# Kernel tuning notes

Hardware: AMD Instinct MI355X
Metric: run time of the kernel (lower is better)

## Reference

```python
import jax, jax.numpy as jnp
import numpy as np


def setup_inputs() -> dict:
    key = jax.random.key(0)
    ks = jax.random.split(key, 5)
    B, T, I, H = 64, 512, 1024, 1024
    s = 1.0 / np.sqrt(H)
    return {
        "x": jax.random.normal(ks[0], (B, T, I), dtype=jnp.float32),
        "w_ih": jax.random.normal(ks[1], (4 * H, I), dtype=jnp.float32) * s,
        "b_ih": jax.random.normal(ks[2], (4 * H,), dtype=jnp.float32) * s,
        "w_hh": jax.random.normal(ks[3], (4 * H, H), dtype=jnp.float32) * s,
        "b_hh": jax.random.normal(ks[4], (4 * H,), dtype=jnp.float32) * s,
    }


def _lstm(x, w_ih, b_ih, w_hh, b_hh):
    B, T, _ = x.shape
    H = w_hh.shape[1]
    # Precompute input projections for all timesteps: [T, B, 4H]
    gx = jnp.einsum("bti,gi->tbg", x, w_ih) + b_ih
    h0 = jnp.zeros((B, H), dtype=x.dtype)
    c0 = jnp.zeros((B, H), dtype=x.dtype)

    def step(carry, g_x):
        h, c = carry
        gates = g_x + h @ w_hh.T + b_hh  # [B, 4H]
        i_lin, f_lin, g_lin, o_lin = jnp.split(gates, 4, axis=-1)
        i = jax.nn.sigmoid(i_lin)
        f = jax.nn.sigmoid(f_lin)
        g = jnp.tanh(g_lin)
        o = jax.nn.sigmoid(o_lin)
        c = f * c + i * g
        h = o * jnp.tanh(c)
        return (h, c), h

    (hT, cT), hs = jax.lax.scan(step, (h0, c0), gx)
    output = jnp.transpose(hs, (1, 0, 2))  # [B, T, H]
    hn = hT[None, :, :]  # [1, B, H]
    cn = cT[None, :, :]
    return output, hn, cn


def reference(x, w_ih, b_ih, w_hh, b_hh):
    return _lstm(x, w_ih, b_ih, w_hh, b_hh)
```

## Files before the change

### kernel.cpp

```cpp
#include <hip/hip_runtime.h>
#include <hip/hip_bf16.h>

#define Bv 64
#define Tv 512
#define Iv 1024
#define Hv 1024
#define G4v 4096
#define BH (Bv * Hv)
#define NHB 64
#define NXB 128
#define NBLK (NHB + NXB)
#define DEPTH 8
#define FSTR 16

typedef __attribute__((ext_vector_type(8))) short bf16x8;
typedef __attribute__((ext_vector_type(4))) float f32x4;

#define LOADC(p)    __hip_atomic_load((p), __ATOMIC_RELAXED, __HIP_MEMORY_SCOPE_AGENT)
#define STOREC(p,v) __hip_atomic_store((p), (v), __ATOMIC_RELAXED, __HIP_MEMORY_SCOPE_AGENT)

__device__ __forceinline__ float sigmoid_f(float v) { return 1.f / (1.f + __expf(-v)); }
__device__ __forceinline__ float tanh_f(float v) { return 1.f - 2.f / (__expf(2.f * v) + 1.f); }

__device__ __forceinline__ void store_short_sc1(void* p, unsigned short v) {
  asm volatile("global_store_short %0, %1, off sc1" :: "v"(p), "v"((unsigned)v) : "memory");
}

__global__ void prep(const float* __restrict__ w_ih, const float* __restrict__ w_hh,
                     const float* __restrict__ b_ih, const float* __restrict__ b_hh,
                     __hip_bfloat16* __restrict__ wbih, __hip_bfloat16* __restrict__ wbhh,
                     float* __restrict__ bias, __hip_bfloat16* __restrict__ hbuf,
                     unsigned* __restrict__ hflag, unsigned* __restrict__ xflag) {
  unsigned i = blockIdx.x * 256u + threadIdx.x;
  wbih[i] = __float2bfloat16(w_ih[i]);
  wbhh[i] = __float2bfloat16(w_hh[i]);
  if (i < (unsigned)G4v) bias[i] = b_ih[i] + b_hh[i];
  if (i < 2u * BH) hbuf[i] = __float2bfloat16(0.f);
  if (i < (unsigned)(4 * NHB * FSTR)) hflag[i] = 0u;
  if (i < (unsigned)(NXB * FSTR)) xflag[i] = 0u;
}

__global__ void __launch_bounds__(256, 1) lstm_main(
    const float* __restrict__ x,
    const __hip_bfloat16* __restrict__ wbih,
    const __hip_bfloat16* __restrict__ wbhh,
    const float* __restrict__ bias,
    __hip_bfloat16* __restrict__ hbuf,
    float* __restrict__ xg,
    float* __restrict__ out,
    unsigned* __restrict__ hflag,
    unsigned* __restrict__ xflag,
    int ring)
{
  extern __shared__ char lds[];

  const int bid  = blockIdx.x;
  const bool is_h = (bid < NHB);
  const int tid  = threadIdx.x;
  const int lane = tid & 63;
  const int wave = tid >> 6;
  const int lrow = lane & 15;
  const int lkg  = lane >> 4;
  const int lk   = lkg * 8;

  const int wg = is_h ? bid : ((bid - NHB) >> 1);
  const int rh = is_h ? 0 : ((bid - NHB) & 1);

  {
    const __hip_bfloat16* wsrc = is_h ? wbhh : wbih;
    for (int c = tid; c < 8192; c += 256) {
      int n   = c >> 7;
      int k16 = c & 127;
      int gc  = ((n >> 4) << 10) + (wg << 4) + (n & 15);
      uint4 v = *(const uint4*)(wsrc + ((size_t)gc << 10) + (k16 << 3));
      unsigned byt = (unsigned)((n << 11) + (k16 << 4)) ^ ((unsigned)(n & 7) << 4);
      *(uint4*)(&lds[byt]) = v;
    }
  }
  __syncthreads();

  if (!is_h) {
    const int j  = bid - NHB;
    const int wr = wave & 1;
    const int wc = wave >> 1;
    const int arow = rh * 32 + wr * 16 + lrow;
    const float* xa = x + (size_t)arow * (Tv * Iv) + lk;

    for (int t = 0; t < Tv; ++t) {
      if (t >= DEPTH) {
        if (wave == 0) {
          const unsigned tgt = (unsigned)(t - DEPTH + 1);
          for (;;) {
            unsigned a0 = LOADC(&hflag[(0 * 64 + lane) * FSTR]);
            unsigned a1 = LOADC(&hflag[(1 * 64 + lane) * FSTR]);
            unsigned a2 = LOADC(&hflag[(2 * 64 + lane) * FSTR]);
            unsigned a3 = LOADC(&hflag[(3 * 64 + lane) * FSTR]);
            if (__all(a0 >= tgt && a1 >= tgt && a2 >= tgt && a3 >= tgt)) break;
            __builtin_amdgcn_s_sleep(4);
          }
        }
        __syncthreads();
        asm volatile("" ::: "memory");
      }
      f32x4 acc[2];
      acc[0] = f32x4{0.f,0.f,0.f,0.f}; acc[1] = f32x4{0.f,0.f,0.f,0.f};
      const float* xt = xa + (size_t)t * Iv;
      #pragma unroll 4
      for (int ks = 0; ks < 32; ++ks) {
        int k0 = (ks << 5) + lk;
        float4 f0 = *(const float4*)(xt + (ks << 5));
        float4 f1 = *(const float4*)(xt + (ks << 5) + 4);
        union { __hip_bfloat16 e[8]; bf16x8 v; } u;
        u.e[0] = __float2bfloat16(f0.x); u.e[1] = __float2bfloat16(f0.y);
        u.e[2] = __float2bfloat16(f0.z); u.e[3] = __float2bfloat16(f0.w);
        u.e[4] = __float2bfloat16(f1.x); u.e[5] = __float2bfloat16(f1.y);
        u.e[6] = __float2bfloat16(f1.z); u.e[7] = __float2bfloat16(f1.w);
        bf16x8 b0, b1;
        {
          int n = wc * 32 + lrow;
          unsigned byt = (unsigned)((n << 11) + (k0 << 1)) ^ ((unsigned)(n & 7) << 4);
          b0 = *(const bf16x8*)(&lds[byt]);
          n += 16;
          byt = (unsigned)((n << 11) + (k0 << 1)) ^ ((unsigned)(n & 7) << 4);
          b1 = *(const bf16x8*)(&lds[byt]);
        }
        acc[0] = __builtin_amdgcn_mfma_f32_16x16x32_bf16(u.v, b0, acc[0], 0, 0, 0);
        acc[1] = __builtin_amdgcn_mfma_f32_16x16x32_bf16(u.v, b1, acc[1], 0, 0, 0);
      }
      float* dst = xg + (size_t)(t & (DEPTH - 1)) * (Bv * G4v);
      for (int nf = 0; nf < 2; ++nf) {
        int gc  = (wc * 2 + nf) * 1024 + (wg << 4) + lrow;
        int row = rh * 32 + wr * 16 + (lkg << 2);
        for (int r = 0; r < 4; ++r)
          STOREC(&dst[(size_t)(row + r) * G4v + gc], acc[nf][r]);
      }
      asm volatile("s_waitcnt vmcnt(0)" ::: "memory");
      __syncthreads();
      if (tid == 0) STOREC(&xflag[j * FSTR], (unsigned)(t + 1));
      __syncthreads();
    }
    return;
  }

  const int s     = wave;
  const int orow0 = s * 16 + (lkg << 2);
  const int ocol  = (wg << 4) + lrow;
  const int ar    = s * 16 + lrow;
  float c_state[4] = {0.f, 0.f, 0.f, 0.f};
  float biasv[4];
  #pragma unroll
  for (int g = 0; g < 4; ++g) biasv[g] = bias[(g << 10) + ocol];
  const unsigned* myxf = &xflag[(2 * wg + (s >> 1)) * FSTR];
  unsigned* myhf = &hflag[(s * 64 + wg) * FSTR];

  for (int t = 0; t < Tv; ++t) {
    for (;;) {
      unsigned hf = LOADC(&hflag[(s * 64 + lane) * FSTR]);
      unsigned xv = LOADC(myxf);
      if (__all(hf >= (unsigned)t && xv >= (unsigned)(t + 1))) break;
      __builtin_amdgcn_s_sleep(1);
    }
    asm volatile("" ::: "memory");
    f32x4 acc[4];
    for (int nf = 0; nf < 4; ++nf) acc[nf] = f32x4{0.f,0.f,0.f,0.f};
    bf16x8 aqv[32];
    if (ring) {
      const char* hrow = (const char*)(hbuf + (size_t)t * BH) + ((size_t)ar << 11) + (lkg << 4);
      #pragma unroll
      for (int ks = 0; ks < 32; ++ks)
        aqv[ks] = *(const bf16x8*)(hrow + (ks << 6));
    } else {
      const unsigned long long* hq =
          (const unsigned long long*)(hbuf + (size_t)(t & 1) * BH) + (size_t)ar * 256 + lkg * 2;
      #pragma unroll
      for (int ks = 0; ks < 32; ++ks) {
        union { unsigned long long q[2]; bf16x8 v; } ua;
        ua.q[0] = LOADC(hq + ks * 8);
        ua.q[1] = LOADC(hq + ks * 8 + 1);
        aqv[ks] = ua.v;
      }
    }
    float xgv[16];
    {
      const float* xgs = xg + (size_t)(t & (DEPTH - 1)) * (Bv * G4v);
      #pragma unroll
      for (int g = 0; g < 4; ++g)
        #pragma unroll
        for (int r = 0; r < 4; ++r)
          xgv[g * 4 + r] = LOADC(xgs + (size_t)(orow0 + r) * G4v + (g << 10) + ocol);
    }
    #pragma unroll
    for (int ks = 0; ks < 32; ++ks) {
      int k0 = (ks << 5) + lk;
      #pragma unroll
      for (int nf = 0; nf < 4; ++nf) {
        int n = nf * 16 + lrow;
        unsigned byt = (unsigned)((n << 11) + (k0 << 1)) ^ ((unsigned)(n & 7) << 4);
        bf16x8 b = *(const bf16x8*)(&lds[byt]);
        acc[nf] = __builtin_amdgcn_mfma_f32_16x16x32_bf16(aqv[ks], b, acc[nf], 0, 0, 0);
      }
    }
    float hv[4];
    #pragma unroll
    for (int r = 0; r < 4; ++r) {
      float g0 = acc[0][r] + xgv[0 + r]  + biasv[0];
      float g1 = acc[1][r] + xgv[4 + r]  + biasv[1];
      float g2 = acc[2][r] + xgv[8 + r]  + biasv[2];
      float g3 = acc[3][r] + xgv[12 + r] + biasv[3];
      float ig = sigmoid_f(g0);
      float fg = sigmoid_f(g1);
      float gg = tanh_f(g2);
      float og = sigmoid_f(g3);
      float cv = fg * c_state[r] + ig * gg;
      c_state[r] = cv;
      hv[r] = og * tanh_f(cv);
    }
    {
      __hip_bfloat16* hs = hbuf
          + (ring ? (size_t)(t + 1) * BH : (size_t)((t + 1) & 1) * BH) + ocol;
      #pragma unroll
      for (int r = 0; r < 4; ++r) {
        __hip_bfloat16 hb = __float2bfloat16(hv[r]);
        store_short_sc1(hs + ((size_t)(orow0 + r) << 10), *(unsigned short*)&hb);
      }
    }
    asm volatile("s_waitcnt vmcnt(0)" ::: "memory");
    if (lane == 0) STOREC(myhf, (unsigned)(t + 1));
    #pragma unroll
    for (int r = 0; r < 4; ++r) {
      float* ow = out + (size_t)(orow0 + r) * (Tv * Hv) + ((size_t)t << 10) + ocol;
      __builtin_nontemporal_store(hv[r], ow);
    }
    if (t == Tv - 1) {
      #pragma unroll
      for (int r = 0; r < 4; ++r) {
        float* hn = out + (size_t)Bv * Tv * Hv + ((size_t)(orow0 + r) << 10) + ocol;
        __builtin_nontemporal_store(hv[r], hn);
        __builtin_nontemporal_store(c_state[r], hn + BH);
      }
    }
  }
}

extern "C" void kernel_launch(void* const* d_in, const int* in_sizes, int n_in,
                              void* d_out, int out_size, void* d_ws, size_t ws_size,
                              hipStream_t stream) {
  const float* x    = (const float*)d_in[0];
  const float* w_ih = (const float*)d_in[1];
  const float* b_ih = (const float*)d_in[2];
  const float* w_hh = (const float*)d_in[3];
  const float* b_hh = (const float*)d_in[4];
  float* out = (float*)d_out;

  char* ws = (char*)d_ws;
  __hip_bfloat16* wbih = (__hip_bfloat16*)(ws);
  __hip_bfloat16* wbhh = (__hip_bfloat16*)(ws + ((size_t)8 << 20));
  float*          bias = (float*)(ws + ((size_t)16 << 20));
  float*          xg   = (float*)(ws + ((size_t)18 << 20));
  unsigned*       hflag= (unsigned*)(ws + ((size_t)26 << 20));
  unsigned*       xflag= (unsigned*)(ws + ((size_t)26 << 20) + 16384);

  const size_t ringBytes = (size_t)(Tv + 1) * BH * 2;
  const size_t needRing  = ((size_t)32 << 20) + ringBytes;
  const int ring = (ws_size >= needRing) ? 1 : 0;
  __hip_bfloat16* hbuf = ring
      ? (__hip_bfloat16*)(ws + ((size_t)32 << 20))
      : (__hip_bfloat16*)(ws + ((size_t)16 << 20) + 65536);

  hipLaunchKernelGGL(prep, dim3(16384), dim3(256), 0, stream,
                     w_ih, w_hh, b_ih, b_hh, wbih, wbhh, bias, hbuf, hflag, xflag);

  const unsigned ldsBytes = 131072u;
  hipFuncSetAttribute((const void*)lstm_main,
                      hipFuncAttributeMaxDynamicSharedMemorySize, (int)ldsBytes);

  const float* xA = x;
  const __hip_bfloat16* wbihA = wbih;
  const __hip_bfloat16* wbhhA = wbhh;
  const float* biasA = bias;
  __hip_bfloat16* hbufA = hbuf;
  float* xgA = xg;
  float* outA = out;
  unsigned* hflagA = hflag;
  unsigned* xflagA = xflag;
  int ringA = ring;
  void* args[10] = {(void*)&xA, (void*)&wbihA, (void*)&wbhhA, (void*)&biasA,
                    (void*)&hbufA, (void*)&xgA, (void*)&outA, (void*)&hflagA,
                    (void*)&xflagA, (void*)&ringA};

  hipError_t lerr = hipLaunchCooperativeKernel((const void*)lstm_main, dim3(NBLK),
                                               dim3(256), args, ldsBytes, stream);
  if (lerr != hipSuccess) {
    (void)hipGetLastError();
    hipLaunchKernelGGL(lstm_main, dim3(NBLK), dim3(256), ldsBytes, stream,
                       xA, wbihA, wbhhA, biasA, hbufA, xgA, outA, hflagA, xflagA, ringA);
  }
}
```

Before: 4.962 ms.

## Replace h-flag polling with sentinel-valued ring buffer data polling

```diff
diff --git a/kernel.cpp b/kernel.cpp
--- a/kernel.cpp
+++ b/kernel.cpp
@@ -12,6 +12,7 @@
 #define NBLK (NHB + NXB)
 #define DEPTH 8
 #define FSTR 16
+#define SENT 0xFF80u
 
 typedef __attribute__((ext_vector_type(8))) short bf16x8;
 typedef __attribute__((ext_vector_type(4))) float f32x4;
@@ -30,12 +31,21 @@
                      const float* __restrict__ b_ih, const float* __restrict__ b_hh,
                      __hip_bfloat16* __restrict__ wbih, __hip_bfloat16* __restrict__ wbhh,
                      float* __restrict__ bias, __hip_bfloat16* __restrict__ hbuf,
-                     unsigned* __restrict__ hflag, unsigned* __restrict__ xflag) {
+                     unsigned* __restrict__ hflag, unsigned* __restrict__ xflag, int ring) {
   unsigned i = blockIdx.x * 256u + threadIdx.x;
   wbih[i] = __float2bfloat16(w_ih[i]);
   wbhh[i] = __float2bfloat16(w_hh[i]);
   if (i < (unsigned)G4v) bias[i] = b_ih[i] + b_hh[i];
-  if (i < 2u * BH) hbuf[i] = __float2bfloat16(0.f);
+  if (ring) {
+    const unsigned NCH = (unsigned)(((size_t)(Tv + 1) * BH) / 8);
+    const uint4 sv = {SENT | (SENT << 16), SENT | (SENT << 16),
+                      SENT | (SENT << 16), SENT | (SENT << 16)};
+    for (unsigned j = i; j < NCH; j += 16384u * 256u)
+      ((uint4*)hbuf)[j] = sv;
+    if (i < (unsigned)(BH / 8)) ((uint4*)hbuf)[i] = uint4{0u, 0u, 0u, 0u};
+  } else {
+    if (i < 2u * BH) hbuf[i] = __float2bfloat16(0.f);
+  }
   if (i < (unsigned)(4 * NHB * FSTR)) hflag[i] = 0u;
   if (i < (unsigned)(NXB * FSTR)) xflag[i] = 0u;
 }
@@ -154,32 +164,53 @@
   unsigned* myhf = &hflag[(s * 64 + wg) * FSTR];
 
   for (int t = 0; t < Tv; ++t) {
-    for (;;) {
-      unsigned hf = LOADC(&hflag[(s * 64 + lane) * FSTR]);
-      unsigned xv = LOADC(myxf);
-      if (__all(hf >= (unsigned)t && xv >= (unsigned)(t + 1))) break;
-      __builtin_amdgcn_s_sleep(1);
-    }
-    asm volatile("" ::: "memory");
-    f32x4 acc[4];
-    for (int nf = 0; nf < 4; ++nf) acc[nf] = f32x4{0.f,0.f,0.f,0.f};
-    bf16x8 aqv[32];
+    unsigned xfv = LOADC(myxf);
+    uint4 av[32];
     if (ring) {
       const char* hrow = (const char*)(hbuf + (size_t)t * BH) + ((size_t)ar << 11) + (lkg << 4);
-      #pragma unroll
-      for (int ks = 0; ks < 32; ++ks)
-        aqv[ks] = *(const bf16x8*)(hrow + (ks << 6));
+      for (;;) {
+        #pragma unroll
+        for (int ks = 0; ks < 32; ++ks)
+          asm volatile("global_load_dwordx4 %0, %1, off sc1"
+                       : "=v"(av[ks]) : "v"(hrow + ((size_t)ks << 6)));
+        asm volatile("s_waitcnt vmcnt(0)" ::: "memory");
+        __builtin_amdgcn_sched_barrier(0);
+        unsigned bad = 0;
+        #pragma unroll
+        for (int ks = 0; ks < 32; ++ks) {
+          bad |= (unsigned)((av[ks].x & 0xFFFFu) == SENT) | (unsigned)((av[ks].x >> 16) == SENT);
+          bad |= (unsigned)((av[ks].y & 0xFFFFu) == SENT) | (unsigned)((av[ks].y >> 16) == SENT);
+          bad |= (unsigned)((av[ks].z & 0xFFFFu) == SENT) | (unsigned)((av[ks].z >> 16) == SENT);
+          bad |= (unsigned)((av[ks].w & 0xFFFFu) == SENT) | (unsigned)((av[ks].w >> 16) == SENT);
+        }
+        if (!__any(bad)) break;
+      }
+      __builtin_amdgcn_sched_barrier(0);
     } else {
+      for (;;) {
+        unsigned hf = LOADC(&hflag[(s * 64 + lane) * FSTR]);
+        if (__all(hf >= (unsigned)t)) break;
+        __builtin_amdgcn_s_sleep(1);
+      }
+      asm volatile("" ::: "memory");
       const unsigned long long* hq =
           (const unsigned long long*)(hbuf + (size_t)(t & 1) * BH) + (size_t)ar * 256 + lkg * 2;
       #pragma unroll
       for (int ks = 0; ks < 32; ++ks) {
-        union { unsigned long long q[2]; bf16x8 v; } ua;
+        union { unsigned long long q[2]; uint4 u; } ua;
         ua.q[0] = LOADC(hq + ks * 8);
         ua.q[1] = LOADC(hq + ks * 8 + 1);
-        aqv[ks] = ua.v;
-      }
-    }
+        av[ks] = ua.u;
+      }
+    }
+    if (xfv < (unsigned)(t + 1)) {
+      for (;;) {
+        xfv = LOADC(myxf);
+        if (__all(xfv >= (unsigned)(t + 1))) break;
+        __builtin_amdgcn_s_sleep(1);
+      }
+    }
+    asm volatile("" ::: "memory");
     float xgv[16];
     {
       const float* xgs = xg + (size_t)(t & (DEPTH - 1)) * (Bv * G4v);
@@ -189,15 +220,19 @@
         for (int r = 0; r < 4; ++r)
           xgv[g * 4 + r] = LOADC(xgs + (size_t)(orow0 + r) * G4v + (g << 10) + ocol);
     }
+    f32x4 acc[4];
+    for (int nf = 0; nf < 4; ++nf) acc[nf] = f32x4{0.f,0.f,0.f,0.f};
     #pragma unroll
     for (int ks = 0; ks < 32; ++ks) {
       int k0 = (ks << 5) + lk;
+      union { uint4 u; bf16x8 v; } ua;
+      ua.u = av[ks];
       #pragma unroll
       for (int nf = 0; nf < 4; ++nf) {
         int n = nf * 16 + lrow;
         unsigned byt = (unsigned)((n << 11) + (k0 << 1)) ^ ((unsigned)(n & 7) << 4);
         bf16x8 b = *(const bf16x8*)(&lds[byt]);
-        acc[nf] = __builtin_amdgcn_mfma_f32_16x16x32_bf16(aqv[ks], b, acc[nf], 0, 0, 0);
+        acc[nf] = __builtin_amdgcn_mfma_f32_16x16x32_bf16(ua.v, b, acc[nf], 0, 0, 0);
       }
     }
     float hv[4];
@@ -224,7 +259,8 @@
         store_short_sc1(hs + ((size_t)(orow0 + r) << 10), *(unsigned short*)&hb);
       }
     }
-    asm volatile("s_waitcnt vmcnt(0)" ::: "memory");
+    if (!ring)
+      asm volatile("s_waitcnt vmcnt(0)" ::: "memory");
     if (lane == 0) STOREC(myhf, (unsigned)(t + 1));
     #pragma unroll
     for (int r = 0; r < 4; ++r) {
@@ -268,7 +304,7 @@
       : (__hip_bfloat16*)(ws + ((size_t)16 << 20) + 65536);
 
   hipLaunchKernelGGL(prep, dim3(16384), dim3(256), 0, stream,
-                     w_ih, w_hh, b_ih, b_hh, wbih, wbhh, bias, hbuf, hflag, xflag);
+                     w_ih, w_hh, b_ih, b_hh, wbih, wbhh, bias, hbuf, hflag, xflag, ring);
 
   const unsigned ldsBytes = 131072u;
   hipFuncSetAttribute((const void*)lstm_main,
```

Measured after the change: 6.574 ms. +32.5%, slower.
